# Optimization experiments

Hardware: AMD Instinct MI355X
Metric: run time of the kernel (lower is better)

Reference implementation:

```python
import jax, jax.numpy as jnp
import numpy as np

N, F_IN, H, C, E, G, OUT = 50000, 128, 4, 64, 800000, 128, 8

def _glorot(key, shape):
    lim = float(np.sqrt(6.0 / (shape[0] + shape[-1] if len(shape) == 2 else shape[-1] + 1)))
    return jax.random.uniform(key, shape, jnp.float32, -lim, lim)

def setup_inputs() -> dict:
    key = jax.random.key(0)
    ks = jax.random.split(key, 12)
    x = jax.random.normal(ks[0], (N, F_IN), jnp.float32)
    edge_index = jax.random.randint(ks[1], (2, E), 0, N, jnp.int64)
    batch = jnp.sort(jax.random.randint(ks[2], (N,), 0, G, jnp.int64))
    return {
        "x": x, "edge_index": edge_index, "batch": batch,
        "W1": _glorot(ks[3], (F_IN, H * C)),
        "a1s": _glorot(ks[4], (H, C)), "a1d": _glorot(ks[5], (H, C)),
        "b1": jnp.zeros((H * C,), jnp.float32),
        "W2": _glorot(ks[6], (H * C, H * C)),
        "a2s": _glorot(ks[7], (H, C)), "a2d": _glorot(ks[8], (H, C)),
        "b2": jnp.zeros((C,), jnp.float32),
        "fc_w": _glorot(ks[9], (C, OUT)),
        "fc_b": jnp.zeros((OUT,), jnp.float32),
    }

def _gat_conv(x, src, dst, W, a_src, a_dst, bias, concat):
    # x: [N, in]; src/dst: [E'] (self-loops already appended, PyG default)
    n = x.shape[0]
    h = (x @ W).reshape(n, H, C)                       # [N, H, C]
    alpha_src = (h * a_src).sum(-1)                    # [N, H]
    alpha_dst = (h * a_dst).sum(-1)                    # [N, H]
    e = alpha_src[src] + alpha_dst[dst]                # [E', H]
    e = jax.nn.leaky_relu(e, 0.2)
    # neighbor softmax grouped by destination node
    m = jax.ops.segment_max(e, dst, num_segments=n)    # [N, H]
    ex = jnp.exp(e - m[dst])
    denom = jax.ops.segment_sum(ex, dst, num_segments=n)
    alpha = ex / (denom[dst] + 1e-16)                  # [E', H]
    msg = h[src] * alpha[:, :, None]                   # [E', H, C]
    out = jax.ops.segment_sum(msg, dst, num_segments=n)  # [N, H, C]
    out = out.reshape(n, H * C) if concat else out.mean(axis=1)
    return out + bias

def reference(x, edge_index, batch, W1, a1s, a1d, b1, W2, a2s, a2d, b2, fc_w, fc_b):
    n = x.shape[0]
    loop = jnp.arange(n, dtype=edge_index.dtype)
    src = jnp.concatenate([edge_index[0], loop])
    dst = jnp.concatenate([edge_index[1], loop])
    h = _gat_conv(x, src, dst, W1, a1s, a1d, b1, concat=True)
    h = jax.nn.elu(h)                                  # activation, dropout p=0
    h = _gat_conv(h, src, dst, W2, a2s, a2d, b2, concat=False)
    # global mean pool over graphs
    sums = jax.ops.segment_sum(h, batch, num_segments=G)
    cnts = jax.ops.segment_sum(jnp.ones((n,), h.dtype), batch, num_segments=G)
    pooled = sums / jnp.maximum(cnts, 1.0)[:, None]    # [G, C]
    return pooled @ fc_w + fc_b                        # [G, OUT]
```

## Files before the change

### kernel.cpp

```cpp
#include <hip/hip_runtime.h>
#include <hip/hip_bf16.h>
#include <cstddef>
#include <cstdint>

#define NN 50000
#define MPAD 50048
#define F_IN 128
#define NH 4
#define NC 64
#define NE 800000
#define NG 128
#define NOUT 8
#define HC 256
#define EP (NE + NN)

typedef unsigned short ushort_t;
typedef _Float16 f16;
typedef __attribute__((ext_vector_type(2))) _Float16 f16x2;
typedef __attribute__((ext_vector_type(8))) _Float16 f16x8;
typedef __attribute__((ext_vector_type(4))) float f32x4;

__device__ __forceinline__ float lrelu02(float x) { return x > 0.0f ? x : 0.2f * x; }
__device__ __forceinline__ float elu1(float x)    { return x > 0.0f ? x : expm1f(x); }

__device__ __forceinline__ ushort_t f2h_bits(float f) {
    f16 h = (f16)f;
    union { f16 h; ushort_t u; } cv; cv.h = h;
    return cv.u;
}
__device__ __forceinline__ uint32_t pack2h(float a, float b) {
    union { f16 h[2]; uint32_t u; } cv;
    cv.h[0] = (f16)a; cv.h[1] = (f16)b;
    return cv.u;
}
__device__ __forceinline__ f16x2 as_h2(uint32_t q) {
    union { uint32_t u; f16x2 h; } cv; cv.u = q;
    return cv.h;
}
__device__ __forceinline__ void h2_unpack(uint32_t q, float& lo, float& hi) {
    union { uint32_t u; f16 h[2]; } cv; cv.u = q;
    lo = (float)cv.h[0];
    hi = (float)cv.h[1];
}

__device__ __forceinline__ void gld16(const void* g, void* l) {
    __builtin_amdgcn_global_load_lds(
        (const __attribute__((address_space(1))) unsigned int*)g,
        (__attribute__((address_space(3))) unsigned int*)l, 16, 0, 0);
}

#define XN4 (NN * F_IN / 4)
#define NW (F_IN * HC + HC * HC)
__global__ void prep_kernel(const int* __restrict__ edst,
                            const float* __restrict__ x,
                            const float* __restrict__ W1,
                            const float* __restrict__ W2,
                            int* __restrict__ deg,
                            f16* __restrict__ xh,
                            f16* __restrict__ w1t, f16* __restrict__ w2t) {
    int idx = blockIdx.x * blockDim.x + threadIdx.x;
    if (idx < EP) {
        int d = (idx < NE) ? edst[idx] : (idx - NE);
        atomicAdd(&deg[d], 1);
        return;
    }
    idx -= EP;
    if (idx < XN4) {
        float4 v = ((const float4*)x)[idx];
        f16 o[4] = {(f16)v.x, (f16)v.y, (f16)v.z, (f16)v.w};
        *(uint2*)(xh + idx * 4) = *(const uint2*)o;
        return;
    }
    idx -= XN4;
    const int n1 = F_IN * HC;
    if (idx < n1) {
        int k = idx / HC, n = idx % HC;
        w1t[n * F_IN + k] = (f16)W1[idx];
    } else if (idx < NW) {
        int i2 = idx - n1;
        int k = i2 / HC, n = i2 % HC;
        w2t[n * HC + k] = (f16)W2[i2];
    }
}

__global__ __launch_bounds__(256) void scan_p1(const int* __restrict__ deg,
                                               int* __restrict__ partials) {
    __shared__ int lds[256];
    int b = blockIdx.x, t = threadIdx.x;
    int i0 = b * 1024 + t * 4;
    int s = 0;
#pragma unroll
    for (int j = 0; j < 4; j++) { int i = i0 + j; if (i < NN) s += deg[i]; }
    lds[t] = s;
    __syncthreads();
    for (int o = 128; o; o >>= 1) { if (t < o) lds[t] += lds[t + o]; __syncthreads(); }
    if (t == 0) partials[b] = lds[0];
}

__global__ __launch_bounds__(256) void scan_p3(const int* __restrict__ deg,
                                               const int* __restrict__ partials,
                                               int* __restrict__ offs) {
    __shared__ int lds[256];
    __shared__ int base_s;
    int b = blockIdx.x, t = threadIdx.x;
    if (t == 0) {
        int s = 0;
        for (int i = 0; i < b; i++) s += partials[i];
        base_s = s;
        if (b == 0) offs[0] = 0;
    }
    int i0 = b * 1024 + t * 4;
    int v[4]; int s = 0;
#pragma unroll
    for (int j = 0; j < 4; j++) { int i = i0 + j; v[j] = (i < NN) ? deg[i] : 0; s += v[j]; }
    lds[t] = s;
    __syncthreads();
    for (int o = 1; o < 256; o <<= 1) {
        int x = (t >= o) ? lds[t - o] : 0;
        __syncthreads();
        lds[t] += x;
        __syncthreads();
    }
    int run = base_s + (lds[t] - s);
#pragma unroll
    for (int j = 0; j < 4; j++) { run += v[j]; int i = i0 + j; if (i < NN) offs[i + 1] = run; }
}

__global__ void edge_fill(const int* __restrict__ esrc, const int* __restrict__ edst,
                          const int* __restrict__ offs, int* __restrict__ fill,
                          int* __restrict__ csr) {
    int e = blockIdx.x * blockDim.x + threadIdx.x;
    if (e >= EP) return;
    int s, d;
    if (e < NE) { s = esrc[e]; d = edst[e]; } else { s = d = e - NE; }
    int pos = offs[d] + atomicAdd(&fill[d], 1);
    csr[pos] = s;
}

__global__ __launch_bounds__(256, 3) void gemm_gat(
        const f16* __restrict__ A, const f16* __restrict__ BT,
        const float* __restrict__ a_s, const float* __restrict__ a_d,
        ushort_t* __restrict__ hf2, float* __restrict__ asrc,
        float* __restrict__ adst, int M, int K) {
    __shared__ alignas(16) char smem[33792];
    f16* lA = (f16*)smem;
    f16* lB = (f16*)smem + 4096;

    int t = threadIdx.x;
    int wave = t >> 6, lane = t & 63;
    int wm = wave >> 1, wn = wave & 1;
    int quad = lane >> 4, l15 = lane & 15;
    int tileM = blockIdx.x * 128;
    int by = blockIdx.y;

    f32x4 acc[4][4];
#pragma unroll
    for (int f = 0; f < 4; f++)
#pragma unroll
        for (int g = 0; g < 4; g++) acc[f][g] = (f32x4){0.f, 0.f, 0.f, 0.f};

    for (int k0 = 0; k0 < K; k0 += 32) {
        __syncthreads();
#pragma unroll
        for (int i = 0; i < 2; i++) {
            int c = wave * 2 + i;
            int row = c * 16 + (lane >> 2);
            int kk = k0 + (lane & 3) * 8;
            gld16(A + (size_t)(tileM + row) * K + kk, &lA[c * 512]);
            gld16(BT + (size_t)(by * 128 + row) * K + kk, &lB[c * 512]);
        }
        __syncthreads();

        f16x8 ah[4], bh[4];
#pragma unroll
        for (int f = 0; f < 4; f++)
            ah[f] = *(const f16x8*)&lA[(wm * 64 + f * 16 + l15) * 32 + quad * 8];
#pragma unroll
        for (int g = 0; g < 4; g++)
            bh[g] = *(const f16x8*)&lB[(wn * 64 + g * 16 + l15) * 32 + quad * 8];
#pragma unroll
        for (int f = 0; f < 4; f++)
#pragma unroll
            for (int g = 0; g < 4; g++)
                acc[f][g] = __builtin_amdgcn_mfma_f32_16x16x32_f16(ah[f], bh[g], acc[f][g], 0, 0, 0);
    }

    int head = (by << 1) | wn;
    float as_v[4], ad_v[4];
#pragma unroll
    for (int g = 0; g < 4; g++) {
        as_v[g] = a_s[head * 64 + g * 16 + l15];
        ad_v[g] = a_d[head * 64 + g * 16 + l15];
    }
#pragma unroll
    for (int f = 0; f < 4; f++) {
#pragma unroll
        for (int r = 0; r < 4; r++) {
            float ps = acc[f][0][r] * as_v[0] + acc[f][1][r] * as_v[1]
                     + acc[f][2][r] * as_v[2] + acc[f][3][r] * as_v[3];
            float pd = acc[f][0][r] * ad_v[0] + acc[f][1][r] * ad_v[1]
                     + acc[f][2][r] * ad_v[2] + acc[f][3][r] * ad_v[3];
#pragma unroll
            for (int o = 1; o < 16; o <<= 1) {
                ps += __shfl_xor(ps, o);
                pd += __shfl_xor(pd, o);
            }
            int row = tileM + wm * 64 + f * 16 + quad * 4 + r;
            if (l15 == 0 && row < M) {
                asrc[row * 4 + head] = ps;
                adst[row * 4 + head] = pd;
            }
        }
    }

    __syncthreads();
    ushort_t* lC2u = (ushort_t*)smem;
    const uint32_t* lC2d = (const uint32_t*)smem;
#pragma unroll
    for (int f = 0; f < 4; f++)
#pragma unroll
        for (int g = 0; g < 4; g++)
#pragma unroll
            for (int r = 0; r < 4; r++)
                lC2u[(wm * 64 + f * 16 + quad * 4 + r) * 132 + (g * 16 + l15) * 2 + wn] =
                    f2h_bits(acc[f][g][r]);
    __syncthreads();
    uint32_t* hb2 = (uint32_t*)hf2;
#pragma unroll
    for (int it = 0; it < 32; it++) {
        int row = wave * 32 + it;
        uint32_t v = lC2d[row * 66 + lane];
        hb2[(size_t)(tileM + row) * 128 + by * 64 + lane] = v;
    }
}

template <int CONCAT>
__global__ __launch_bounds__(256) void gat_agg(const ushort_t* __restrict__ hf2,
                                               const float* __restrict__ asrc,
                                               const float* __restrict__ adst,
                                               const int* __restrict__ offs,
                                               const int* __restrict__ csr,
                                               const float* __restrict__ bias,
                                               f16* __restrict__ oh,
                                               float* __restrict__ of) {
    __shared__ uint2 lw[4][64];
    int wave = threadIdx.x >> 6, lane = threadIdx.x & 63;
    int node = blockIdx.x * 4 + wave;
    if (node >= NN) return;
    int start = offs[node];
    int deg = offs[node + 1] - start;
    float4 ad = *(const float4*)(adst + node * 4);

    float w0, w1, w2, w3;
    float m0, m1, m2, m3, i0, i1, i2, i3;
    int msrc = 0;

    if (deg <= 64) {
        float t0 = -1e30f, t1 = -1e30f, t2 = -1e30f, t3 = -1e30f;
        if (lane < deg) {
            int sidx = csr[start + lane];
            float4 as = *(const float4*)(asrc + sidx * 4);
            t0 = lrelu02(as.x + ad.x);
            t1 = lrelu02(as.y + ad.y);
            t2 = lrelu02(as.z + ad.z);
            t3 = lrelu02(as.w + ad.w);
            msrc = sidx;
        }
        m0 = t0; m1 = t1; m2 = t2; m3 = t3;
#pragma unroll
        for (int o = 1; o < 64; o <<= 1) {
            m0 = fmaxf(m0, __shfl_xor(m0, o));
            m1 = fmaxf(m1, __shfl_xor(m1, o));
            m2 = fmaxf(m2, __shfl_xor(m2, o));
            m3 = fmaxf(m3, __shfl_xor(m3, o));
        }
        w0 = __expf(t0 - m0);
        w1 = __expf(t1 - m1);
        w2 = __expf(t2 - m2);
        w3 = __expf(t3 - m3);
        float s0 = w0, s1 = w1, s2 = w2, s3 = w3;
#pragma unroll
        for (int o = 1; o < 64; o <<= 1) {
            s0 += __shfl_xor(s0, o);
            s1 += __shfl_xor(s1, o);
            s2 += __shfl_xor(s2, o);
            s3 += __shfl_xor(s3, o);
        }
        i0 = 1.0f / (s0 + 1e-16f);
        i1 = 1.0f / (s1 + 1e-16f);
        i2 = 1.0f / (s2 + 1e-16f);
        i3 = 1.0f / (s3 + 1e-16f);
        w0 *= i0; w1 *= i1; w2 *= i2; w3 *= i3;
    } else {
        m0 = m1 = m2 = m3 = -1e30f;
        float s0 = 0.f, s1 = 0.f, s2 = 0.f, s3 = 0.f;
        float e0 = 0.f, e1 = 0.f, e2 = 0.f, e3 = 0.f;
        for (int j = lane; j < deg; j += 64) {
            int sidx = csr[start + j];
            float4 as = *(const float4*)(asrc + sidx * 4);
            float t0 = lrelu02(as.x + ad.x);
            float t1 = lrelu02(as.y + ad.y);
            float t2 = lrelu02(as.z + ad.z);
            float t3 = lrelu02(as.w + ad.w);
            if (j == lane) { e0 = t0; e1 = t1; e2 = t2; e3 = t3; msrc = sidx; }
            float nm;
            nm = fmaxf(m0, t0); s0 = s0 * __expf(m0 - nm) + __expf(t0 - nm); m0 = nm;
            nm = fmaxf(m1, t1); s1 = s1 * __expf(m1 - nm) + __expf(t1 - nm); m1 = nm;
            nm = fmaxf(m2, t2); s2 = s2 * __expf(m2 - nm) + __expf(t2 - nm); m2 = nm;
            nm = fmaxf(m3, t3); s3 = s3 * __expf(m3 - nm) + __expf(t3 - nm); m3 = nm;
        }
        for (int o = 32; o; o >>= 1) {
            float om, os, nm;
            om = __shfl_xor(m0, o); os = __shfl_xor(s0, o);
            nm = fmaxf(m0, om); s0 = s0 * __expf(m0 - nm) + os * __expf(om - nm); m0 = nm;
            om = __shfl_xor(m1, o); os = __shfl_xor(s1, o);
            nm = fmaxf(m1, om); s1 = s1 * __expf(m1 - nm) + os * __expf(om - nm); m1 = nm;
            om = __shfl_xor(m2, o); os = __shfl_xor(s2, o);
            nm = fmaxf(m2, om); s2 = s2 * __expf(m2 - nm) + os * __expf(om - nm); m2 = nm;
            om = __shfl_xor(m3, o); os = __shfl_xor(s3, o);
            nm = fmaxf(m3, om); s3 = s3 * __expf(m3 - nm) + os * __expf(om - nm); m3 = nm;
        }
        i0 = 1.0f / (s0 + 1e-16f);
        i1 = 1.0f / (s1 + 1e-16f);
        i2 = 1.0f / (s2 + 1e-16f);
        i3 = 1.0f / (s3 + 1e-16f);
        w0 = __expf(e0 - m0) * i0;
        w1 = __expf(e1 - m1) * i1;
        w2 = __expf(e2 - m2) * i2;
        w3 = __expf(e3 - m3) * i3;
    }

    lw[wave][lane] = (uint2){pack2h(w0, w1), pack2h(w2, w3)};

    int hp = lane >> 5;
    const uint32_t* lwu = (const uint32_t*)&lw[wave][0];
    float aE0 = 0.f, aO0 = 0.f, aE1 = 0.f, aO1 = 0.f;
    const uint32_t* hb = (const uint32_t*)hf2 + lane * 2;
    int jmax = deg < 64 ? deg : 64;
#pragma unroll 16
    for (int j = 0; j < jmax; j++) {
        int sidx = __builtin_amdgcn_readlane(msrc, j);
        f16x2 wh = as_h2(lwu[j * 2 + hp]);
        uint2 q = *(const uint2*)(hb + (size_t)sidx * 128);
        f16x2 qx = as_h2(q.x), qy = as_h2(q.y);
        aE0 += (float)qx[0] * (float)wh[0];
        aO0 += (float)qx[1] * (float)wh[1];
        aE1 += (float)qy[0] * (float)wh[0];
        aO1 += (float)qy[1] * (float)wh[1];
    }
    for (int j = 64; j < deg; j++) {
        int sidx = csr[start + j];
        float4 as = *(const float4*)(asrc + sidx * 4);
        float u0 = __expf(lrelu02(as.x + ad.x) - m0) * i0;
        float u1 = __expf(lrelu02(as.y + ad.y) - m1) * i1;
        float u2 = __expf(lrelu02(as.z + ad.z) - m2) * i2;
        float u3 = __expf(lrelu02(as.w + ad.w) - m3) * i3;
        float ue = hp ? u2 : u0;
        float uo = hp ? u3 : u1;
        uint2 q = *(const uint2*)(hb + (size_t)sidx * 128);
        float xl, xh2, yl, yh;
        h2_unpack(q.x, xl, xh2);
        h2_unpack(q.y, yl, yh);
        aE0 += ue * xl;
        aO0 += uo * xh2;
        aE1 += ue * yl;
        aO1 += uo * yh;
    }

    int c0 = (lane & 31) * 2;
    int he = hp * 2, ho = hp * 2 + 1;
    if (CONCAT) {
        size_t base = (size_t)node * HC;
        float vE0 = elu1(aE0 + bias[he * 64 + c0]);
        float vE1 = elu1(aE1 + bias[he * 64 + c0 + 1]);
        float vO0 = elu1(aO0 + bias[ho * 64 + c0]);
        float vO1 = elu1(aO1 + bias[ho * 64 + c0 + 1]);
        f16 pe[2] = {(f16)vE0, (f16)vE1};
        f16 po[2] = {(f16)vO0, (f16)vO1};
        *(uint32_t*)(oh + base + he * 64 + c0) = *(const uint32_t*)pe;
        *(uint32_t*)(oh + base + ho * 64 + c0) = *(const uint32_t*)po;
    } else {
        float s0 = aE0 + aO0;
        float s1 = aE1 + aO1;
        s0 += __shfl_xor(s0, 32);
        s1 += __shfl_xor(s1, 32);
        if (hp == 0) {
            float2 v = {0.25f * s0 + bias[c0], 0.25f * s1 + bias[c0 + 1]};
            *(float2*)(of + (size_t)node * NC + c0) = v;
        }
    }
}

__global__ __launch_bounds__(256) void pool_kernel(const float* __restrict__ out2,
                                                   const int* __restrict__ batch,
                                                   float* __restrict__ pool,
                                                   float* __restrict__ cnt) {
    int gw = (blockIdx.x * blockDim.x + threadIdx.x) >> 6;
    int lane = threadIdx.x & 63;
    int start = gw * 16;
    if (start >= NN) return;
    int end = start + 16 < NN ? start + 16 : NN;
    int curg = batch[start];
    float acc = 0.f; int run = 0;
    for (int node = start; node < end; node++) {
        int g = batch[node];
        if (g != curg) {
            atomicAdd(&pool[curg * 64 + lane], acc);
            if (lane == 0) atomicAdd(&cnt[curg], (float)run);
            curg = g; acc = 0.f; run = 0;
        }
        acc += out2[(size_t)node * NC + lane];
        run++;
    }
    atomicAdd(&pool[curg * 64 + lane], acc);
    if (lane == 0) atomicAdd(&cnt[curg], (float)run);
}

__global__ void fc_kernel(const float* __restrict__ pool, const float* __restrict__ cnt,
                          const float* __restrict__ fc_w, const float* __restrict__ fc_b,
                          float* __restrict__ out) {
    int idx = blockIdx.x * blockDim.x + threadIdx.x;
    if (idx >= NG * NOUT) return;
    int g = idx >> 3, o = idx & 7;
    float inv = 1.0f / fmaxf(cnt[g], 1.0f);
    float s = 0.f;
#pragma unroll
    for (int c = 0; c < 64; c++) s += pool[g * 64 + c] * fc_w[c * 8 + o];
    out[idx] = s * inv + fc_b[o];
}

extern "C" void kernel_launch(void* const* d_in, const int* in_sizes, int n_in,
                              void* d_out, int out_size, void* d_ws, size_t ws_size,
                              hipStream_t stream) {
    const float* x    = (const float*)d_in[0];
    const int*   ei   = (const int*)d_in[1];
    const int*   batch= (const int*)d_in[2];
    const float* W1   = (const float*)d_in[3];
    const float* a1s  = (const float*)d_in[4];
    const float* a1d  = (const float*)d_in[5];
    const float* b1   = (const float*)d_in[6];
    const float* W2   = (const float*)d_in[7];
    const float* a2s  = (const float*)d_in[8];
    const float* a2d  = (const float*)d_in[9];
    const float* b2   = (const float*)d_in[10];
    const float* fc_w = (const float*)d_in[11];
    const float* fc_b = (const float*)d_in[12];
    float* out = (float*)d_out;

    char* p = (char*)d_ws;
    auto alloc = [&](size_t bytes) -> char* {
        char* r = p; p += (bytes + 255) & ~(size_t)255; return r;
    };
    int*   deg     = (int*)alloc((size_t)NN * 4);
    int*   fill    = (int*)alloc((size_t)NN * 4);
    float* pool    = (float*)alloc((size_t)NG * 64 * 4);
    float* cnt     = (float*)alloc((size_t)NG * 4);
    size_t zero_bytes = (size_t)(p - (char*)d_ws);
    int*   offs    = (int*)alloc((size_t)(NN + 1) * 4);
    int*   partials= (int*)alloc(64 * 4);
    int*   csr     = (int*)alloc((size_t)EP * 4);
    float* asrc    = (float*)alloc((size_t)NN * 4 * 4);
    float* adst    = (float*)alloc((size_t)NN * 4 * 4);
    ushort_t* hf2  = (ushort_t*)alloc((size_t)MPAD * HC * 2);
    f16*   xh      = (f16*)alloc((size_t)MPAD * F_IN * 2);
    f16*   act     = (f16*)alloc((size_t)MPAD * HC * 2);
    f16*   w1t     = (f16*)alloc((size_t)HC * F_IN * 2);
    f16*   w2t     = (f16*)alloc((size_t)HC * HC * 2);
    float* out2    = (float*)xh;

    hipMemsetAsync(d_ws, 0, zero_bytes, stream);

    int prep_n = EP + XN4 + NW;
    prep_kernel<<<(prep_n + 255) / 256, 256, 0, stream>>>(
        ei + NE, x, W1, W2, deg, xh, w1t, w2t);
    scan_p1<<<49, 256, 0, stream>>>(deg, partials);
    scan_p3<<<49, 256, 0, stream>>>(deg, partials, offs);
    edge_fill<<<(EP + 255) / 256, 256, 0, stream>>>(ei, ei + NE, offs, fill, csr);

    dim3 gg((NN + 127) / 128, HC / 128);
    int nb4 = (NN + 3) / 4;

    gemm_gat<<<gg, 256, 0, stream>>>(xh, w1t, a1s, a1d, hf2, asrc, adst, NN, F_IN);
    gat_agg<1><<<nb4, 256, 0, stream>>>(hf2, asrc, adst, offs, csr, b1, act, nullptr);
    gemm_gat<<<gg, 256, 0, stream>>>(act, w2t, a2s, a2d, hf2, asrc, adst, NN, HC);
    gat_agg<0><<<nb4, 256, 0, stream>>>(hf2, asrc, adst, offs, csr, b2, nullptr, out2);
    pool_kernel<<<((NN + 15) / 16 + 3) / 4, 256, 0, stream>>>(out2, batch, pool, cnt);
    fc_kernel<<<(NG * NOUT + 255) / 256, 256, 0, stream>>>(pool, cnt, fc_w, fc_b, out);
}
```

Before: 397.2 us.

## Prefetch neighbor features with 8-deep ring buffer and widen GEMM K-tile

Measured after the change: 519.9 us. 1.31x slower.

```diff
diff --git a/kernel.cpp b/kernel.cpp
--- a/kernel.cpp
+++ b/kernel.cpp
@@ -144,7 +144,7 @@
         float* __restrict__ adst, int M, int K) {
     __shared__ alignas(16) char smem[33792];
     f16* lA = (f16*)smem;
-    f16* lB = (f16*)smem + 4096;
+    f16* lB = (f16*)smem + 8192;
 
     int t = threadIdx.x;
     int wave = t >> 6, lane = t & 63;
@@ -159,30 +159,33 @@
 #pragma unroll
         for (int g = 0; g < 4; g++) acc[f][g] = (f32x4){0.f, 0.f, 0.f, 0.f};
 
-    for (int k0 = 0; k0 < K; k0 += 32) {
+    for (int k0 = 0; k0 < K; k0 += 64) {
         __syncthreads();
 #pragma unroll
-        for (int i = 0; i < 2; i++) {
-            int c = wave * 2 + i;
-            int row = c * 16 + (lane >> 2);
-            int kk = k0 + (lane & 3) * 8;
+        for (int i = 0; i < 4; i++) {
+            int c = wave * 4 + i;
+            int row = c * 8 + (lane >> 3);
+            int kk = k0 + (lane & 7) * 8;
             gld16(A + (size_t)(tileM + row) * K + kk, &lA[c * 512]);
             gld16(BT + (size_t)(by * 128 + row) * K + kk, &lB[c * 512]);
         }
         __syncthreads();
 
-        f16x8 ah[4], bh[4];
-#pragma unroll
-        for (int f = 0; f < 4; f++)
-            ah[f] = *(const f16x8*)&lA[(wm * 64 + f * 16 + l15) * 32 + quad * 8];
-#pragma unroll
-        for (int g = 0; g < 4; g++)
-            bh[g] = *(const f16x8*)&lB[(wn * 64 + g * 16 + l15) * 32 + quad * 8];
-#pragma unroll
-        for (int f = 0; f < 4; f++)
+#pragma unroll
+        for (int h = 0; h < 2; h++) {
+            f16x8 ah[4], bh[4];
+#pragma unroll
+            for (int f = 0; f < 4; f++)
+                ah[f] = *(const f16x8*)&lA[(wm * 64 + f * 16 + l15) * 64 + h * 32 + quad * 8];
 #pragma unroll
             for (int g = 0; g < 4; g++)
-                acc[f][g] = __builtin_amdgcn_mfma_f32_16x16x32_f16(ah[f], bh[g], acc[f][g], 0, 0, 0);
+                bh[g] = *(const f16x8*)&lB[(wn * 64 + g * 16 + l15) * 64 + h * 32 + quad * 8];
+#pragma unroll
+            for (int f = 0; f < 4; f++)
+#pragma unroll
+                for (int g = 0; g < 4; g++)
+                    acc[f][g] = __builtin_amdgcn_mfma_f32_16x16x32_f16(ah[f], bh[g], acc[f][g], 0, 0, 0);
+        }
     }
 
     int head = (by << 1) | wn;
@@ -337,19 +340,40 @@
     float aE0 = 0.f, aO0 = 0.f, aE1 = 0.f, aO1 = 0.f;
     const uint32_t* hb = (const uint32_t*)hf2 + lane * 2;
     int jmax = deg < 64 ? deg : 64;
-#pragma unroll 16
-    for (int j = 0; j < jmax; j++) {
-        int sidx = __builtin_amdgcn_readlane(msrc, j);
+
+    uint2 q[8];
+#pragma unroll
+    for (int k = 0; k < 8; k++) {
+        if (k < jmax) {
+            int s0 = __builtin_amdgcn_readlane(msrc, k);
+            q[k] = *(const uint2*)(hb + (size_t)s0 * 128);
+        }
+    }
+    int j = 0;
+#pragma unroll 8
+    for (; j + 8 < jmax; j++) {
+        uint2 cur = q[j & 7];
+        int sn = __builtin_amdgcn_readlane(msrc, j + 8);
+        q[j & 7] = *(const uint2*)(hb + (size_t)sn * 128);
         f16x2 wh = as_h2(lwu[j * 2 + hp]);
-        uint2 q = *(const uint2*)(hb + (size_t)sidx * 128);
-        f16x2 qx = as_h2(q.x), qy = as_h2(q.y);
+        f16x2 qx = as_h2(cur.x), qy = as_h2(cur.y);
         aE0 += (float)qx[0] * (float)wh[0];
         aO0 += (float)qx[1] * (float)wh[1];
         aE1 += (float)qy[0] * (float)wh[0];
         aO1 += (float)qy[1] * (float)wh[1];
     }
-    for (int j = 64; j < deg; j++) {
-        int sidx = csr[start + j];
+#pragma unroll 8
+    for (; j < jmax; j++) {
+        uint2 cur = q[j & 7];
+        f16x2 wh = as_h2(lwu[j * 2 + hp]);
+        f16x2 qx = as_h2(cur.x), qy = as_h2(cur.y);
+        aE0 += (float)qx[0] * (float)wh[0];
+        aO0 += (float)qx[1] * (float)wh[1];
+        aE1 += (float)qy[0] * (float)wh[0];
+        aO1 += (float)qy[1] * (float)wh[1];
+    }
+    for (int jj = 64; jj < deg; jj++) {
+        int sidx = csr[start + jj];
         float4 as = *(const float4*)(asrc + sidx * 4);
         float u0 = __expf(lrelu02(as.x + ad.x) - m0) * i0;
         float u1 = __expf(lrelu02(as.y + ad.y) - m1) * i1;
@@ -357,10 +381,10 @@
         float u3 = __expf(lrelu02(as.w + ad.w) - m3) * i3;
         float ue = hp ? u2 : u0;
         float uo = hp ? u3 : u1;
-        uint2 q = *(const uint2*)(hb + (size_t)sidx * 128);
+        uint2 qq = *(const uint2*)(hb + (size_t)sidx * 128);
         float xl, xh2, yl, yh;
-        h2_unpack(q.x, xl, xh2);
-        h2_unpack(q.y, yl, yh);
+        h2_unpack(qq.x, xl, xh2);
+        h2_unpack(qq.y, yl, yh);
         aE0 += ue * xl;
         aO0 += uo * xh2;
         aE1 += ue * yl;
```
